# Performance work log

Hardware: AMD Instinct MI355X
Metric: run time of the kernel (lower is better)

## Reference

```python
import jax, jax.numpy as jnp
import numpy as np
from jax import lax

# Module hyperparameters (from LIF_BTN.__init__ defaults)
V_TH = 1.0    # firing threshold
TAU = 0.5     # membrane leak factor
ALPHA = 1.0   # surrogate-gradient sharpness

T, B, N = 32, 32, 32768


@jax.custom_vjp
def spike(u):
    # Heaviside spike: fires when membrane potential crosses threshold (u = m - v_th)
    return (u >= 0.0).astype(u.dtype)


def _spike_fwd(u):
    return spike(u), u


def _spike_bwd(u, g):
    # Sigmoid surrogate gradient: d/du sigmoid(alpha*u) = alpha*s*(1-s)
    s = jax.nn.sigmoid(ALPHA * u)
    return (g * (ALPHA * s * (1.0 - s)),)


spike.defvjp(_spike_fwd, _spike_bwd)


def setup_inputs() -> dict:
    key = jax.random.key(0)
    x = jax.random.normal(key, (T, B, N), dtype=jnp.float32)
    return {"x": x}


def reference(x):
    # LIF membrane scan over time (time-major x: [T, B, N]):
    #   m[t] = tau * v[t-1] + x[t]
    #   y[t] = heaviside(m[t] - v_th)       (surrogate grad in backward)
    #   v[t] = m[t] * (1 - y[t])            (hard reset to 0 after spike)
    def step(v, x_t):
        m = TAU * v + x_t
        y = spike(m - V_TH)
        v_next = m * (1.0 - y)
        return v_next, y

    v0 = jnp.zeros(x.shape[1:], dtype=x.dtype)
    _, y_seq = lax.scan(step, v0, x)
    return y_seq
```

## Files before the change

kernel.cpp:

```cpp
#include <hip/hip_runtime.h>


typedef float f32x2 __attribute__((ext_vector_type(2)));

#define T_STEPS 32
#define CHUNK 16
#define TAU 0.5f
#define V_TH 1.0f

__global__ __launch_bounds__(256) void lif_btn_kernel(
    const f32x2* __restrict__ x, f32x2* __restrict__ y, int n2) {
    int idx = blockIdx.x * blockDim.x + threadIdx.x;
    if (idx >= n2) return;

    const f32x2* xp = x + idx;
    f32x2* yp = y + idx;

    f32x2 v;
    v.x = 0.f; v.y = 0.f;

    f32x2 cur[CHUNK], nxt[CHUNK];

    #pragma unroll
    for (int i = 0; i < CHUNK; ++i)
        cur[i] = xp[(size_t)i * n2];

    #pragma unroll
    for (int c = 0; c < T_STEPS / CHUNK; ++c) {
        if (c + 1 < T_STEPS / CHUNK) {
            #pragma unroll
            for (int i = 0; i < CHUNK; ++i)
                nxt[i] = xp[(size_t)((c + 1) * CHUNK + i) * n2];
        }
        #pragma unroll
        for (int i = 0; i < CHUNK; ++i) {
            f32x2 m, out;
            m.x = TAU * v.x + cur[i].x;
            m.y = TAU * v.y + cur[i].y;
            out.x = (m.x >= V_TH) ? 1.f : 0.f;
            out.y = (m.y >= V_TH) ? 1.f : 0.f;
            v.x = (m.x >= V_TH) ? 0.f : m.x;
            v.y = (m.y >= V_TH) ? 0.f : m.y;
            __builtin_nontemporal_store(out, yp + (size_t)(c * CHUNK + i) * n2);
        }
        #pragma unroll
        for (int i = 0; i < CHUNK; ++i)
            cur[i] = nxt[i];
    }
}

extern "C" void kernel_launch(void* const* d_in, const int* in_sizes, int n_in,
                              void* d_out, int out_size, void* d_ws, size_t ws_size,
                              hipStream_t stream) {
    const float* x = (const float*)d_in[0];
    float* y = (float*)d_out;

    int total = in_sizes[0];
    int per_t = total / T_STEPS;
    int n2 = per_t / 2;

    const int block = 256;
    int grid = (n2 + block - 1) / block;
    lif_btn_kernel<<<grid, block, 0, stream>>>(
        (const f32x2*)x, (f32x2*)y, n2);
}
```

Baseline: 54.64 us.

## Replace chunked double-buffer with rolling ring-buffer prefetch of depth eight

New measurement: 46.29 us. 15.3% less time.

```diff
diff --git a/kernel.cpp b/kernel.cpp
--- a/kernel.cpp
+++ b/kernel.cpp
@@ -4,7 +4,7 @@
 typedef float f32x2 __attribute__((ext_vector_type(2)));
 
 #define T_STEPS 32
-#define CHUNK 16
+#define DEPTH 8
 #define TAU 0.5f
 #define V_TH 1.0f
 
@@ -19,33 +19,26 @@
     f32x2 v;
     v.x = 0.f; v.y = 0.f;
 
-    f32x2 cur[CHUNK], nxt[CHUNK];
+    f32x2 buf[DEPTH];
 
     #pragma unroll
-    for (int i = 0; i < CHUNK; ++i)
-        cur[i] = xp[(size_t)i * n2];
+    for (int t = 0; t < DEPTH; ++t)
+        buf[t] = xp[(size_t)t * n2];
 
     #pragma unroll
-    for (int c = 0; c < T_STEPS / CHUNK; ++c) {
-        if (c + 1 < T_STEPS / CHUNK) {
-            #pragma unroll
-            for (int i = 0; i < CHUNK; ++i)
-                nxt[i] = xp[(size_t)((c + 1) * CHUNK + i) * n2];
-        }
-        #pragma unroll
-        for (int i = 0; i < CHUNK; ++i) {
-            f32x2 m, out;
-            m.x = TAU * v.x + cur[i].x;
-            m.y = TAU * v.y + cur[i].y;
-            out.x = (m.x >= V_TH) ? 1.f : 0.f;
-            out.y = (m.y >= V_TH) ? 1.f : 0.f;
-            v.x = (m.x >= V_TH) ? 0.f : m.x;
-            v.y = (m.y >= V_TH) ? 0.f : m.y;
-            __builtin_nontemporal_store(out, yp + (size_t)(c * CHUNK + i) * n2);
-        }
-        #pragma unroll
-        for (int i = 0; i < CHUNK; ++i)
-            cur[i] = nxt[i];
+    for (int t = 0; t < T_STEPS; ++t) {
+        f32x2 xt = buf[t & (DEPTH - 1)];
+        if (t + DEPTH < T_STEPS)
+            buf[t & (DEPTH - 1)] = xp[(size_t)(t + DEPTH) * n2];
+
+        f32x2 m, out;
+        m.x = TAU * v.x + xt.x;
+        m.y = TAU * v.y + xt.y;
+        out.x = (m.x >= V_TH) ? 1.f : 0.f;
+        out.y = (m.y >= V_TH) ? 1.f : 0.f;
+        v.x = (m.x >= V_TH) ? 0.f : m.x;
+        v.y = (m.y >= V_TH) ? 0.f : m.y;
+        __builtin_nontemporal_store(out, yp + (size_t)t * n2);
     }
 }
 
```
